# Optimization experiments

Measured on AMD Instinct MI355X. Metric: run time of the kernel, lower is better.

## Reference

```python
import jax, jax.numpy as jnp
import numpy as np

DEGREE = 3
NUM_KNOTS = 64
NUM_NEURONS = 256
BATCH = 4096


def _extended_knots():
    """Replicates knots_distribution + sklearn SplineTransformer knot extension.

    Base knots (nk-2 values): linspace(-0.002,-0.001,dg) ++ linspace(0,1,nk-2*dg-2)
    ++ linspace(1.001,1.002,dg). sklearn then pads `degree` knots on each side
    using the boundary knot spacing, giving M = nk - 2 + 2*degree knots and
    M - degree - 1 = nk + degree - 3 = nk basis functions (degree==3).
    """
    dg, nk = DEGREE, NUM_KNOTS
    base = np.concatenate([
        np.linspace(-0.002, -0.001, dg),
        np.linspace(0.0, 1.0, nk - 2 * dg - 2),
        np.linspace(1.001, 1.002, dg),
    ])
    dist_lo = base[1] - base[0]
    dist_hi = base[-1] - base[-2]
    left = base[0] - dist_lo * np.arange(dg, 0, -1)
    right = base[-1] + dist_hi * np.arange(1, dg + 1)
    return jnp.asarray(np.concatenate([left, base, right]), dtype=jnp.float32)


def _bspline_basis(x, t, degree):
    """Vectorized Cox-de Boor recursion.

    x: (..., ) samples; t: (M,) extended knots.
    Returns basis of shape (..., M - degree - 1).
    """
    xe = x[..., None]
    # order-0: indicator of half-open knot intervals, shape (..., M-1)
    B = ((t[:-1] <= xe) & (xe < t[1:])).astype(x.dtype)
    for k in range(1, degree + 1):
        d1 = t[k:-1] - t[:-k - 1]   # (M-k-1,)
        d2 = t[k + 1:] - t[1:-k]    # (M-k-1,)
        w1 = jnp.where(d1 != 0, (xe - t[:-k - 1]) / jnp.where(d1 != 0, d1, 1.0), 0.0)
        w2 = jnp.where(d2 != 0, (t[k + 1:] - xe) / jnp.where(d2 != 0, d2, 1.0), 0.0)
        B = w1 * B[..., :-1] + w2 * B[..., 1:]
    return B


def setup_inputs() -> dict:
    key = jax.random.key(0)
    k1, k2, k3 = jax.random.split(key, 3)
    x = jax.random.uniform(k1, (BATCH, NUM_NEURONS), dtype=jnp.float32)
    control_p = jax.random.normal(k2, (NUM_KNOTS, NUM_NEURONS), dtype=jnp.float32)
    bias = jax.random.normal(k3, (NUM_NEURONS,), dtype=jnp.float32)
    return {"x": x, "control_p": control_p, "bias": bias}


def reference(x, control_p, bias):
    t = _extended_knots()
    # Same B-spline knot vector for every feature, so compute basis jointly:
    # basis[b, f, k] == (torch) basises.permute(1,2,0)[b, k, f]
    basis = _bspline_basis(x, t, DEGREE)          # (batch, F, num_knots)
    out = jnp.einsum('bfk,kf->bf', basis, control_p) + bias
    return out
```

## Files before the change

### kernel.cpp

```cpp
#include <hip/hip_runtime.h>

#define NF 256
#define NK 64
#define ROWS_PER_BLOCK 8


__global__ __launch_bounds__(256, 2) void bspline_kernel(
    const float* __restrict__ x,
    const float* __restrict__ cp,
    const float* __restrict__ bias,
    float* __restrict__ out)
{
    __shared__ float4 cpl4[NK * NF / 4];
    float* cpl = reinterpret_cast<float*>(cpl4);

    const int tid = threadIdx.x;

    {
        const float4* cp4 = reinterpret_cast<const float4*>(cp);
#pragma unroll
        for (int it = 0; it < NK * NF / 4 / 256; ++it)
            cpl4[tid + 256 * it] = cp4[tid + 256 * it];
    }

    const float bv = bias[tid];
    __syncthreads();

    const int r0 = blockIdx.x * ROWS_PER_BLOCK;
    constexpr float inv55 = 1.0f / 55.0f;

#pragma unroll
    for (int j = 0; j < ROWS_PER_BLOCK; ++j) {
        const float xx = x[(r0 + j) * NF + tid];

        float jf = floorf(xx * 55.0f);
        jf = fminf(fmaxf(jf, 0.0f), 54.0f);
        const int ji = (int)jf;

        const float t_im2 = fmaxf(fmaf(jf, 5e-4f, -1.5e-3f), (jf - 2.0f) * inv55);
        const float t_im1 = fmaxf(fmaf(jf, 5e-4f, -1.0e-3f), (jf - 1.0f) * inv55);
        const float t_i   = jf * inv55;
        const float t_ip1 = (jf + 1.0f) * inv55;
        const float t_ip2 = fminf((jf + 2.0f) * inv55, fmaf(jf, 5e-4f, 0.974f));
        const float t_ip3 = fminf((jf + 3.0f) * inv55, fmaf(jf, 5e-4f, 0.9745f));

        const float l1 = xx - t_i,   r1 = t_ip1 - xx;
        const float l2 = xx - t_im1, r2 = t_ip2 - xx;
        const float l3 = xx - t_im2, r3 = t_ip3 - xx;

        const float rd11 = __builtin_amdgcn_rcpf(l1 + r1);
        const float rd21 = __builtin_amdgcn_rcpf(l2 + r1);
        const float rd22 = __builtin_amdgcn_rcpf(l1 + r2);
        const float rd31 = __builtin_amdgcn_rcpf(l3 + r1);
        const float rd32 = __builtin_amdgcn_rcpf(l2 + r2);
        const float rd33 = __builtin_amdgcn_rcpf(l1 + r3);

        float temp = rd11;
        float N0 = r1 * temp;
        float N1 = l1 * temp;
        temp = N0 * rd21; N0 = r1 * temp; float saved = l2 * temp;
        temp = N1 * rd22; N1 = fmaf(r2, temp, saved); float N2 = l1 * temp;
        temp = N0 * rd31; N0 = r1 * temp; saved = l3 * temp;
        temp = N1 * rd32; N1 = fmaf(r2, temp, saved); saved = l2 * temp;
        temp = N2 * rd33; N2 = fmaf(r3, temp, saved); const float N3 = l1 * temp;

        const float* c = &cpl[(ji + 3) * NF + tid];
        float acc = fmaf(N0, c[0 * NF], bv);
        acc = fmaf(N1, c[1 * NF], acc);
        acc = fmaf(N2, c[2 * NF], acc);
        acc = fmaf(N3, c[3 * NF], acc);

        out[(r0 + j) * NF + tid] = acc;
    }
}

extern "C" void kernel_launch(void* const* d_in, const int* in_sizes, int n_in,
                              void* d_out, int out_size, void* d_ws, size_t ws_size,
                              hipStream_t stream) {
    const float* x    = (const float*)d_in[0];
    const float* cp   = (const float*)d_in[1];
    const float* bias = (const float*)d_in[2];
    float* out = (float*)d_out;

    const int batch = in_sizes[0] / NF;
    const int grid = batch / ROWS_PER_BLOCK;
    bspline_kernel<<<grid, 256, 0, stream>>>(x, cp, bias, out);
}
```

Baseline: 60.97 us.

## Tile blocks over feature groups to shrink per-block control-point staging

Each block now covers 64 features by 32 rows instead of all 256 features by 8 rows, so it stages only a quarter of the control-point table into LDS (16 KB instead of 64 KB). This cuts redundant global-to-LDS traffic per output and allows more blocks per CU. All eight x values are loaded into registers before the LDS fill so their latency overlaps with it. Rows are still written as 256-byte contiguous segments per wavefront, and the grid keeps the same block count.

Result: no change. 60.71 us (-0.4%).

```diff
diff --git a/kernel.cpp b/kernel.cpp
--- a/kernel.cpp
+++ b/kernel.cpp
@@ -2,7 +2,8 @@
 
 #define NF 256
 #define NK 64
-#define ROWS_PER_BLOCK 8
+#define FPB 64
+#define RPB 32
 
 
 __global__ __launch_bounds__(256, 2) void bspline_kernel(
@@ -11,27 +12,42 @@
     const float* __restrict__ bias,
     float* __restrict__ out)
 {
-    __shared__ float4 cpl4[NK * NF / 4];
+    __shared__ float4 cpl4[NK * FPB / 4];
     float* cpl = reinterpret_cast<float*>(cpl4);
 
-    const int tid = threadIdx.x;
+    const int tid  = threadIdx.x;
+    const int ff   = tid & (FPB - 1);
+    const int rsub = tid >> 6;
+    const int fg   = blockIdx.x & 3;
+    const int rg   = blockIdx.x >> 2;
+    const int f0   = fg * FPB;
+    const int r0   = rg * RPB;
+
+    const float* xp = x + (r0 + rsub) * NF + f0 + ff;
+    float xv[8];
+#pragma unroll
+    for (int it = 0; it < 8; ++it)
+        xv[it] = xp[it * 4 * NF];
 
     {
         const float4* cp4 = reinterpret_cast<const float4*>(cp);
+        const int fb4 = f0 >> 2;
 #pragma unroll
-        for (int it = 0; it < NK * NF / 4 / 256; ++it)
-            cpl4[tid + 256 * it] = cp4[tid + 256 * it];
+        for (int s = 0; s < 4; ++s) {
+            const int idx = tid + 256 * s;
+            const int k   = idx >> 4;
+            const int c4  = idx & 15;
+            cpl4[idx] = cp4[k * (NF / 4) + fb4 + c4];
+        }
     }
-
-    const float bv = bias[tid];
+    const float bv = bias[f0 + ff];
     __syncthreads();
 
-    const int r0 = blockIdx.x * ROWS_PER_BLOCK;
     constexpr float inv55 = 1.0f / 55.0f;
 
 #pragma unroll
-    for (int j = 0; j < ROWS_PER_BLOCK; ++j) {
-        const float xx = x[(r0 + j) * NF + tid];
+    for (int it = 0; it < 8; ++it) {
+        const float xx = xv[it];
 
         float jf = floorf(xx * 55.0f);
         jf = fminf(fmaxf(jf, 0.0f), 54.0f);
@@ -64,13 +80,13 @@
         temp = N1 * rd32; N1 = fmaf(r2, temp, saved); saved = l2 * temp;
         temp = N2 * rd33; N2 = fmaf(r3, temp, saved); const float N3 = l1 * temp;
 
-        const float* c = &cpl[(ji + 3) * NF + tid];
-        float acc = fmaf(N0, c[0 * NF], bv);
-        acc = fmaf(N1, c[1 * NF], acc);
-        acc = fmaf(N2, c[2 * NF], acc);
-        acc = fmaf(N3, c[3 * NF], acc);
+        const float* c = &cpl[(ji + 3) * FPB + ff];
+        float acc = fmaf(N0, c[0 * FPB], bv);
+        acc = fmaf(N1, c[1 * FPB], acc);
+        acc = fmaf(N2, c[2 * FPB], acc);
+        acc = fmaf(N3, c[3 * FPB], acc);
 
-        out[(r0 + j) * NF + tid] = acc;
+        out[(r0 + rsub + it * 4) * NF + f0 + ff] = acc;
     }
 }
 
@@ -83,6 +99,6 @@
     float* out = (float*)d_out;
 
     const int batch = in_sizes[0] / NF;
-    const int grid = batch / ROWS_PER_BLOCK;
+    const int grid = (batch / RPB) * (NF / FPB);
     bspline_kernel<<<grid, 256, 0, stream>>>(x, cp, bias, out);
 }
```
